# Kernel optimization log

Hardware: AMD Instinct MI355X
Metric: run time of the kernel (lower is better)

Reference implementation:

```python
import jax, jax.numpy as jnp
import numpy as np

B, IN_DIM, EXP_DIM, E = 16384, 256, 128, 8  # batch, input_dim, expert_dim, expert_num


def setup_inputs() -> dict:
    key = jax.random.key(0)
    ks = jax.random.split(key, 12)
    s_in = 1.0 / np.sqrt(IN_DIM)
    return {
        "x_a": jax.random.normal(ks[0], (B, IN_DIM), jnp.float32),
        "x_b": jax.random.normal(ks[1], (B, IN_DIM), jnp.float32),
        "x_share": jax.random.normal(ks[2], (B, IN_DIM), jnp.float32),
        # expert banks: [E, IN_DIM, EXP_DIM] weights, [E, EXP_DIM] bias
        "Wa": jax.random.uniform(ks[3], (E, IN_DIM, EXP_DIM), jnp.float32, -s_in, s_in),
        "ba": jax.random.uniform(ks[4], (E, EXP_DIM), jnp.float32, -s_in, s_in),
        "Wb": jax.random.uniform(ks[5], (E, IN_DIM, EXP_DIM), jnp.float32, -s_in, s_in),
        "bb": jax.random.uniform(ks[6], (E, EXP_DIM), jnp.float32, -s_in, s_in),
        "Ws": jax.random.uniform(ks[7], (E, IN_DIM, EXP_DIM), jnp.float32, -s_in, s_in),
        "bs": jax.random.uniform(ks[8], (E, EXP_DIM), jnp.float32, -s_in, s_in),
        # gate projections (bias=False): num single-output linears == one [num, IN_DIM] matrix
        "Ga": jax.random.uniform(ks[9], (2 * E, IN_DIM), jnp.float32, -s_in, s_in),
        "Gb": jax.random.uniform(ks[10], (2 * E, IN_DIM), jnp.float32, -s_in, s_in),
        "Gs": jax.random.uniform(ks[11], (3 * E, IN_DIM), jnp.float32, -s_in, s_in),
    }


def _experts(x, W, b):
    # batched dense stack: [B,IN] x [E,IN,D] -> [B,E,D]
    return jnp.einsum("bi,eid->bed", x, W) + b[None, :, :]


def _gate(x, G, experts):
    # logits [B, num]; softmax over experts; weighted sum over expert axis
    w = jax.nn.softmax(x @ G.T, axis=1)
    return jnp.einsum("be,bed->bd", w, experts)


def reference(x_a, x_b, x_share, Wa, ba, Wb, bb, Ws, bs, Ga, Gb, Gs):
    ea = _experts(x_a, Wa, ba)          # [B,E,D]
    eb = _experts(x_b, Wb, bb)          # [B,E,D]
    es = _experts(x_share, Ws, bs)      # [B,E,D]
    out_a = _gate(x_a, Ga, jnp.concatenate([ea, es], axis=1))
    out_b = _gate(x_b, Gb, jnp.concatenate([eb, es], axis=1))
    out_s = _gate(x_share, Gs, jnp.concatenate([ea, eb, es], axis=1))
    return (out_a, out_b, out_s)
```

## Files before the change

### kernel.cpp

```cpp
#include <hip/hip_runtime.h>
#include <stdint.h>

#define BATCH 16384
#define INDIM 256
#define DDIM  128
#define NEXP  8
#define ROWS  64

typedef __bf16 bfv8  __attribute__((ext_vector_type(8)));
typedef float  f32x4 __attribute__((ext_vector_type(4)));

__global__ void prep_kernel(const float* __restrict__ Wa, const float* __restrict__ Wb,
                            const float* __restrict__ Ws, const float* __restrict__ Ga,
                            const float* __restrict__ Gb, const float* __restrict__ Gs,
                            __bf16* __restrict__ wp, __bf16* __restrict__ gp) {
    int t = blockIdx.x * 256 + threadIdx.x;
    const int NW = 3 * 8 * 8 * 8 * 64;
    if (t < NW) {
        int lane = t & 63, nt = (t >> 6) & 7, kt = (t >> 9) & 7, e = (t >> 12) & 7, st = t >> 15;
        const float* W = (st == 0) ? Wa : (st == 1) ? Wb : Ws;
        int d  = nt * 16 + (lane & 15);
        int i0 = kt * 32 + (lane >> 4) * 8;
        __bf16* o = wp + (size_t)t * 8;
#pragma unroll
        for (int j = 0; j < 8; j++)
            o[j] = (__bf16)W[(size_t)(e * 256 + i0 + j) * 128 + d];
    } else if (t < NW + 2048) {
        int t2 = t - NW;
        int lane = t2 & 63, nt = (t2 >> 6) & 3, kt = t2 >> 8;
        int g  = nt * 16 + (lane & 15);
        int k0 = kt * 32 + (lane >> 4) * 8;
        __bf16* o = gp + (size_t)t2 * 8;
#pragma unroll
        for (int j = 0; j < 8; j++) {
            int k = k0 + j;
            float v = 0.f;
            if (g < 16)      v = Ga[g * 256 + k];
            else if (g < 32) v = Gb[(g - 16) * 256 + k];
            else if (g < 56) v = Gs[(g - 32) * 256 + k];
            o[j] = (__bf16)v;
        }
    }
}

__device__ __forceinline__ void load_afr(const float* __restrict__ x, int rb,
                                         int l16, int quad, bfv8 afr[2][8]) {
#pragma unroll
    for (int mt = 0; mt < 2; mt++) {
        const float* xr = x + (size_t)(rb + mt * 16 + l16) * INDIM;
#pragma unroll
        for (int kt = 0; kt < 8; kt++) {
            f32x4 lo = *(const f32x4*)(xr + kt * 32 + quad * 8);
            f32x4 hi = *(const f32x4*)(xr + kt * 32 + quad * 8 + 4);
            bfv8 a;
            a[0] = (__bf16)lo[0]; a[1] = (__bf16)lo[1]; a[2] = (__bf16)lo[2]; a[3] = (__bf16)lo[3];
            a[4] = (__bf16)hi[0]; a[5] = (__bf16)hi[1]; a[6] = (__bf16)hi[2]; a[7] = (__bf16)hi[3];
            afr[mt][kt] = a;
        }
    }
}

__launch_bounds__(512, 2)
__global__ void ple_kernel(const float* __restrict__ xa, const float* __restrict__ xb,
                           const float* __restrict__ xs,
                           const float* __restrict__ ba, const float* __restrict__ bb,
                           const float* __restrict__ bs,
                           const __bf16* __restrict__ wp, const __bf16* __restrict__ gp,
                           float* __restrict__ out) {
    __shared__ float lgt[ROWS * 64];
    __shared__ float wT[64 * ROWS];

    const int tid  = threadIdx.x;
    const int w    = tid >> 6;
    const int lane = tid & 63;
    const int quad = lane >> 4;
    const int l16  = lane & 15;
    const int r0   = blockIdx.x * ROWS;

    bfv8 afr[2][8];

    {
        const int nt  = w >> 1;
        const int mh  = (w & 1) * 32;
        const float* x = (nt == 0) ? xa : (nt == 1) ? xb : xs;
        load_afr(x, r0 + mh, l16, quad, afr);
        f32x4 acc[2];
#pragma unroll
        for (int mt = 0; mt < 2; mt++) { f32x4 z = {0.f, 0.f, 0.f, 0.f}; acc[mt] = z; }
#pragma unroll
        for (int kt = 0; kt < 8; kt++) {
            bfv8 g = *(const bfv8*)(gp + ((size_t)(kt * 4 + nt) * 64 + lane) * 8);
#pragma unroll
            for (int mt = 0; mt < 2; mt++)
                acc[mt] = __builtin_amdgcn_mfma_f32_16x16x32_bf16(afr[mt][kt], g, acc[mt], 0, 0, 0);
        }
#pragma unroll
        for (int mt = 0; mt < 2; mt++)
#pragma unroll
            for (int r = 0; r < 4; r++)
                lgt[(mh + mt * 16 + quad * 4 + r) * 64 + nt * 16 + l16] = acc[mt][r];
    }
    __syncthreads();

    if (tid < ROWS) {
        const float* L = lgt + tid * 64;
#pragma unroll
        for (int gi = 0; gi < 3; gi++) {
            const int base = (gi == 0) ? 0 : (gi == 1 ? 16 : 32);
            const int cnt  = (gi == 2) ? 24 : 16;
            float m = -1e30f;
            for (int k = 0; k < cnt; k++) m = fmaxf(m, L[base + k]);
            float s = 0.f;
            for (int k = 0; k < cnt; k++) s += __expf(L[base + k] - m);
            float inv = 1.f / s;
            for (int k = 0; k < cnt; k++) wT[(base + k) * ROWS + tid] = __expf(L[base + k] - m) * inv;
        }
    }
    __syncthreads();

    const int wr = w >> 2;
    const int wc = w & 3;
    const int mb = wr * 32;

    float o[3][2][2][4];
#pragma unroll
    for (int oi = 0; oi < 3; oi++)
#pragma unroll
        for (int mt = 0; mt < 2; mt++)
#pragma unroll
            for (int ntl = 0; ntl < 2; ntl++)
#pragma unroll
                for (int r = 0; r < 4; r++) o[oi][mt][ntl][r] = 0.f;

#define FOLD(oi, gbase)                                                                \
    {                                                                                  \
        _Pragma("unroll")                                                              \
        for (int mt = 0; mt < 2; mt++) {                                               \
            f32x4 wv = *(const f32x4*)(wT + (gbase + eb) * ROWS + mb + mt * 16 + quad * 4); \
            _Pragma("unroll")                                                          \
            for (int ntl = 0; ntl < 2; ntl++)                                          \
                _Pragma("unroll")                                                      \
                for (int r = 0; r < 4; r++)                                            \
                    o[oi][mt][ntl][r] += wv[r] * acc[mt][ntl][r];                      \
        }                                                                              \
    }

    const __bf16* colb = wp + (size_t)(2 * wc) * 512 + (size_t)lane * 8;

    bfv8 cb[4][2];
#pragma unroll
    for (int i = 0; i < 4; i++) {
        cb[i][0] = *(const bfv8*)(colb + (size_t)i * 4096);
        cb[i][1] = *(const bfv8*)(colb + (size_t)i * 4096 + 512);
    }

#pragma unroll
    for (int st = 0; st < 3; st++) {
        const float* x    = (st == 0) ? xa : (st == 1) ? xb : xs;
        const float* bias = (st == 0) ? ba : (st == 1) ? bb : bs;
        load_afr(x, r0 + mb, l16, quad, afr);

#pragma unroll 1
        for (int eb = 0; eb < NEXP; eb++) {
            float b0 = bias[eb * 128 + wc * 32 + l16];
            float b1 = bias[eb * 128 + wc * 32 + 16 + l16];

            f32x4 acc[2][2];
#pragma unroll
            for (int mt = 0; mt < 2; mt++)
#pragma unroll
                for (int ntl = 0; ntl < 2; ntl++) { f32x4 z = {0.f, 0.f, 0.f, 0.f}; acc[mt][ntl] = z; }

#pragma unroll
            for (int kt = 0; kt < 8; kt++) {
                const int sl = kt & 3;
                acc[0][0] = __builtin_amdgcn_mfma_f32_16x16x32_bf16(afr[0][kt], cb[sl][0], acc[0][0], 0, 0, 0);
                acc[1][0] = __builtin_amdgcn_mfma_f32_16x16x32_bf16(afr[1][kt], cb[sl][0], acc[1][0], 0, 0, 0);
                acc[0][1] = __builtin_amdgcn_mfma_f32_16x16x32_bf16(afr[0][kt], cb[sl][1], acc[0][1], 0, 0, 0);
                acc[1][1] = __builtin_amdgcn_mfma_f32_16x16x32_bf16(afr[1][kt], cb[sl][1], acc[1][1], 0, 0, 0);
                if (kt < 4 || st < 2 || eb < NEXP - 1) {
                    size_t gpf = (size_t)(st * 64 + eb * 8 + kt + 4) * 4096;
                    cb[sl][0] = *(const bfv8*)(colb + gpf);
                    cb[sl][1] = *(const bfv8*)(colb + gpf + 512);
                }
            }

#pragma unroll
            for (int mt = 0; mt < 2; mt++)
#pragma unroll
                for (int r = 0; r < 4; r++) { acc[mt][0][r] += b0; acc[mt][1][r] += b1; }

            if (st == 0)      { FOLD(0, 0);  FOLD(2, 32); }
            else if (st == 1) { FOLD(1, 16); FOLD(2, 40); }
            else              { FOLD(0, 8);  FOLD(1, 24); FOLD(2, 48); }
        }
    }
#undef FOLD

#pragma unroll
    for (int oi = 0; oi < 3; oi++) {
        float* ob = out + (size_t)oi * BATCH * DDIM;
#pragma unroll
        for (int mt = 0; mt < 2; mt++)
#pragma unroll
            for (int r = 0; r < 4; r++) {
                int row = r0 + mb + mt * 16 + quad * 4 + r;
#pragma unroll
                for (int ntl = 0; ntl < 2; ntl++)
                    ob[(size_t)row * DDIM + wc * 32 + ntl * 16 + l16] = o[oi][mt][ntl][r];
            }
    }
}

extern "C" void kernel_launch(void* const* d_in, const int* in_sizes, int n_in,
                              void* d_out, int out_size, void* d_ws, size_t ws_size,
                              hipStream_t stream) {
    const float* xa = (const float*)d_in[0];
    const float* xb = (const float*)d_in[1];
    const float* xs = (const float*)d_in[2];
    const float* Wa = (const float*)d_in[3];
    const float* ba = (const float*)d_in[4];
    const float* Wb = (const float*)d_in[5];
    const float* bb = (const float*)d_in[6];
    const float* Ws = (const float*)d_in[7];
    const float* bs = (const float*)d_in[8];
    const float* Ga = (const float*)d_in[9];
    const float* Gb = (const float*)d_in[10];
    const float* Gs = (const float*)d_in[11];

    __bf16* wp = (__bf16*)d_ws;
    __bf16* gp = wp + 3 * 8 * 8 * 8 * 64 * 8;

    prep_kernel<<<392, 256, 0, stream>>>(Wa, Wb, Ws, Ga, Gb, Gs, wp, gp);
    ple_kernel<<<BATCH / ROWS, 512, 0, stream>>>(xa, xb, xs, ba, bb, bs, wp, gp, (float*)d_out);
}
```

Measured before the change: 170.0 us.

## Warp-specialize expert GEMM with async global-to-LDS producer waves and double buffering

Adds two producer waves per block that stream each expert's bf16 weight tile into a double-buffered LDS area using global_load_lds. Consumer waves synchronize with the producers through workgroup-scope ready/done flags and read MFMA B operands from LDS instead of prefetching them into registers from global memory. The logit buffer now aliases the first LDS buffer. The aim is to overlap weight fetch with MFMA work and free registers. In exchange, LDS use rises to about 144KB per block, and spin-wait synchronization adds latency and the risk of stalls.

```diff
diff --git a/kernel.cpp b/kernel.cpp
--- a/kernel.cpp
+++ b/kernel.cpp
@@ -60,15 +60,23 @@
     }
 }
 
-__launch_bounds__(512, 2)
+__device__ __forceinline__ void async_load16(const __bf16* g, __bf16* l) {
+    __builtin_amdgcn_global_load_lds(
+        (const __attribute__((address_space(1))) uint32_t*)g,
+        (__attribute__((address_space(3))) uint32_t*)l, 16, 0, 0);
+}
+
+__launch_bounds__(640, 2)
 __global__ void ple_kernel(const float* __restrict__ xa, const float* __restrict__ xb,
                            const float* __restrict__ xs,
                            const float* __restrict__ ba, const float* __restrict__ bb,
                            const float* __restrict__ bs,
                            const __bf16* __restrict__ wp, const __bf16* __restrict__ gp,
                            float* __restrict__ out) {
-    __shared__ float lgt[ROWS * 64];
-    __shared__ float wT[64 * ROWS];
+    __shared__ __bf16 Bbuf[2][32768];
+    __shared__ float  wT[64 * ROWS];
+    __shared__ int    ready[24];
+    __shared__ int    done[24];
 
     const int tid  = threadIdx.x;
     const int w    = tid >> 6;
@@ -77,28 +85,28 @@
     const int l16  = lane & 15;
     const int r0   = blockIdx.x * ROWS;
 
-    bfv8 afr[2][8];
-
-    {
-        const int nt  = w >> 1;
-        const int mh  = (w & 1) * 32;
+    float* lgt = (float*)&Bbuf[0][0];
+
+    if (tid < 24) { ready[tid] = 0; done[tid] = 0; }
+
+    if (w < 8) {
+        const int nt = w >> 1;
+        const int mh = (w & 1) * 32;
         const float* x = (nt == 0) ? xa : (nt == 1) ? xb : xs;
+        bfv8 afr[2][8];
         load_afr(x, r0 + mh, l16, quad, afr);
-        f32x4 acc[2];
-#pragma unroll
-        for (int mt = 0; mt < 2; mt++) { f32x4 z = {0.f, 0.f, 0.f, 0.f}; acc[mt] = z; }
+        f32x4 acc0 = {0.f, 0.f, 0.f, 0.f}, acc1 = {0.f, 0.f, 0.f, 0.f};
 #pragma unroll
         for (int kt = 0; kt < 8; kt++) {
             bfv8 g = *(const bfv8*)(gp + ((size_t)(kt * 4 + nt) * 64 + lane) * 8);
-#pragma unroll
-            for (int mt = 0; mt < 2; mt++)
-                acc[mt] = __builtin_amdgcn_mfma_f32_16x16x32_bf16(afr[mt][kt], g, acc[mt], 0, 0, 0);
-        }
-#pragma unroll
-        for (int mt = 0; mt < 2; mt++)
-#pragma unroll
-            for (int r = 0; r < 4; r++)
-                lgt[(mh + mt * 16 + quad * 4 + r) * 64 + nt * 16 + l16] = acc[mt][r];
+            acc0 = __builtin_amdgcn_mfma_f32_16x16x32_bf16(afr[0][kt], g, acc0, 0, 0, 0);
+            acc1 = __builtin_amdgcn_mfma_f32_16x16x32_bf16(afr[1][kt], g, acc1, 0, 0, 0);
+        }
+#pragma unroll
+        for (int r = 0; r < 4; r++) {
+            lgt[(mh + quad * 4 + r) * 64 + nt * 16 + l16]      = acc0[r];
+            lgt[(mh + 16 + quad * 4 + r) * 64 + nt * 16 + l16] = acc1[r];
+        }
     }
     __syncthreads();
 
@@ -117,6 +125,27 @@
         }
     }
     __syncthreads();
+
+    if (w >= 8) {
+        const int pid = w - 8;
+#pragma unroll 1
+        for (int g = pid; g < 24; g += 2) {
+            if (g >= 2) {
+                while (__hip_atomic_load(&done[g - 2], __ATOMIC_ACQUIRE,
+                                         __HIP_MEMORY_SCOPE_WORKGROUP) < 8)
+                    __builtin_amdgcn_s_sleep(2);
+            }
+            const __bf16* gsrc = wp + (size_t)g * 32768 + (size_t)lane * 8;
+            __bf16* ldst = &Bbuf[g & 1][0];
+#pragma unroll
+            for (int c = 0; c < 64; c++)
+                async_load16(gsrc + (size_t)c * 512, ldst + c * 512);
+            __asm__ volatile("s_waitcnt vmcnt(0)" ::: "memory");
+            __hip_atomic_store(&ready[g], 1, __ATOMIC_RELEASE,
+                               __HIP_MEMORY_SCOPE_WORKGROUP);
+        }
+        return;
+    }
 
     const int wr = w >> 2;
     const int wc = w & 3;
@@ -145,55 +174,53 @@
         }                                                                              \
     }
 
-    const __bf16* colb = wp + (size_t)(2 * wc) * 512 + (size_t)lane * 8;
-
-    bfv8 cb[4][2];
-#pragma unroll
-    for (int i = 0; i < 4; i++) {
-        cb[i][0] = *(const bfv8*)(colb + (size_t)i * 4096);
-        cb[i][1] = *(const bfv8*)(colb + (size_t)i * 4096 + 512);
-    }
-
-#pragma unroll
-    for (int st = 0; st < 3; st++) {
-        const float* x    = (st == 0) ? xa : (st == 1) ? xb : xs;
+    bfv8 afr[2][8];
+
+#pragma unroll 1
+    for (int g = 0; g < 24; g++) {
+        const int st = g >> 3;
+        const int eb = g & 7;
+        if ((g & 7) == 0) {
+            const float* x = (st == 0) ? xa : (st == 1) ? xb : xs;
+            load_afr(x, r0 + mb, l16, quad, afr);
+        }
+        while (__hip_atomic_load(&ready[g], __ATOMIC_ACQUIRE,
+                                 __HIP_MEMORY_SCOPE_WORKGROUP) == 0)
+            __builtin_amdgcn_s_sleep(1);
+
+        const __bf16* bbase = &Bbuf[g & 1][0] + (size_t)(2 * wc) * 512 + (size_t)lane * 8;
+
+        f32x4 acc[2][2];
+#pragma unroll
+        for (int mt = 0; mt < 2; mt++)
+#pragma unroll
+            for (int ntl = 0; ntl < 2; ntl++) { f32x4 z = {0.f, 0.f, 0.f, 0.f}; acc[mt][ntl] = z; }
+
+#pragma unroll
+        for (int kt = 0; kt < 8; kt++) {
+            bfv8 c0 = *(const bfv8*)(bbase + (size_t)kt * 4096);
+            bfv8 c1 = *(const bfv8*)(bbase + (size_t)kt * 4096 + 512);
+            acc[0][0] = __builtin_amdgcn_mfma_f32_16x16x32_bf16(afr[0][kt], c0, acc[0][0], 0, 0, 0);
+            acc[1][0] = __builtin_amdgcn_mfma_f32_16x16x32_bf16(afr[1][kt], c0, acc[1][0], 0, 0, 0);
+            acc[0][1] = __builtin_amdgcn_mfma_f32_16x16x32_bf16(afr[0][kt], c1, acc[0][1], 0, 0, 0);
+            acc[1][1] = __builtin_amdgcn_mfma_f32_16x16x32_bf16(afr[1][kt], c1, acc[1][1], 0, 0, 0);
+        }
+
+        if (lane == 0)
+            __hip_atomic_fetch_add(&done[g], 1, __ATOMIC_RELEASE,
+                                   __HIP_MEMORY_SCOPE_WORKGROUP);
+
         const float* bias = (st == 0) ? ba : (st == 1) ? bb : bs;
-        load_afr(x, r0 + mb, l16, quad, afr);
-
-#pragma unroll 1
-        for (int eb = 0; eb < NEXP; eb++) {
-            float b0 = bias[eb * 128 + wc * 32 + l16];
-            float b1 = bias[eb * 128 + wc * 32 + 16 + l16];
-
-            f32x4 acc[2][2];
-#pragma unroll
-            for (int mt = 0; mt < 2; mt++)
-#pragma unroll
-                for (int ntl = 0; ntl < 2; ntl++) { f32x4 z = {0.f, 0.f, 0.f, 0.f}; acc[mt][ntl] = z; }
-
-#pragma unroll
-            for (int kt = 0; kt < 8; kt++) {
-                const int sl = kt & 3;
-                acc[0][0] = __builtin_amdgcn_mfma_f32_16x16x32_bf16(afr[0][kt], cb[sl][0], acc[0][0], 0, 0, 0);
-                acc[1][0] = __builtin_amdgcn_mfma_f32_16x16x32_bf16(afr[1][kt], cb[sl][0], acc[1][0], 0, 0, 0);
-                acc[0][1] = __builtin_amdgcn_mfma_f32_16x16x32_bf16(afr[0][kt], cb[sl][1], acc[0][1], 0, 0, 0);
-                acc[1][1] = __builtin_amdgcn_mfma_f32_16x16x32_bf16(afr[1][kt], cb[sl][1], acc[1][1], 0, 0, 0);
-                if (kt < 4 || st < 2 || eb < NEXP - 1) {
-                    size_t gpf = (size_t)(st * 64 + eb * 8 + kt + 4) * 4096;
-                    cb[sl][0] = *(const bfv8*)(colb + gpf);
-                    cb[sl][1] = *(const bfv8*)(colb + gpf + 512);
-                }
-            }
-
-#pragma unroll
-            for (int mt = 0; mt < 2; mt++)
-#pragma unroll
-                for (int r = 0; r < 4; r++) { acc[mt][0][r] += b0; acc[mt][1][r] += b1; }
-
-            if (st == 0)      { FOLD(0, 0);  FOLD(2, 32); }
-            else if (st == 1) { FOLD(1, 16); FOLD(2, 40); }
-            else              { FOLD(0, 8);  FOLD(1, 24); FOLD(2, 48); }
-        }
+        float b0 = bias[eb * 128 + wc * 32 + l16];
+        float b1 = bias[eb * 128 + wc * 32 + 16 + l16];
+#pragma unroll
+        for (int mt = 0; mt < 2; mt++)
+#pragma unroll
+            for (int r = 0; r < 4; r++) { acc[mt][0][r] += b0; acc[mt][1][r] += b1; }
+
+        if (st == 0)      { FOLD(0, 0);  FOLD(2, 32); }
+        else if (st == 1) { FOLD(1, 16); FOLD(2, 40); }
+        else              { FOLD(0, 8);  FOLD(1, 24); FOLD(2, 48); }
     }
 #undef FOLD
 
@@ -232,5 +259,5 @@
     __bf16* gp = wp + 3 * 8 * 8 * 8 * 64 * 8;
 
     prep_kernel<<<392, 256, 0, stream>>>(Wa, Wb, Ws, Ga, Gb, Gs, wp, gp);
-    ple_kernel<<<BATCH / ROWS, 512, 0, stream>>>(xa, xb, xs, ba, bb, bs, wp, gp, (float*)d_out);
-}
+    ple_kernel<<<BATCH / ROWS, 640, 0, stream>>>(xa, xb, xs, ba, bb, bs, wp, gp, (float*)d_out);
+}
```

After: 194.2 us. 14.3% more time.
